# Optimization experiments

Measured on AMD Instinct MI355X. Metric: run time of the kernel, lower is better.

## Reference

```python
import jax, jax.numpy as jnp
import numpy as np

B, CIN, COUT, H, W = 8, 64, 64, 96, 96
K = 3
PAD = 1
BN_EPS = 1e-5


def conv2d(x, w, b):
    # plain 3x3 conv, stride 1, pad 1 (NCHW / OIHW)
    y = jax.lax.conv_general_dilated(
        x, w, window_strides=(1, 1), padding=[(PAD, PAD), (PAD, PAD)],
        dimension_numbers=("NCHW", "OIHW", "NCHW"))
    return y + b[None, :, None, None]


def setup_inputs() -> dict:
    key = jax.random.key(0)
    ks = jax.random.split(key, 6)
    s = 0.05  # small init so offsets stay near the regular grid (matches DCN zero-ish init)
    return {
        "x": jax.random.normal(ks[0], (B, CIN, H, W), jnp.float32),
        "offset_w": jax.random.normal(ks[1], (2 * K * K, CIN, K, K), jnp.float32) * s,
        "offset_b": jnp.zeros((2 * K * K,), jnp.float32),
        "mod_w": jax.random.normal(ks[2], (K * K, CIN, K, K), jnp.float32) * s,
        "mod_b": jnp.zeros((K * K,), jnp.float32),
        "weight": jax.random.normal(ks[3], (COUT, CIN, K, K), jnp.float32) * s,
        "bias": jax.random.normal(ks[4], (COUT,), jnp.float32) * s,
        "bn_gamma": jnp.ones((COUT,), jnp.float32),
        "bn_beta": jnp.zeros((COUT,), jnp.float32),
        "bn_mean": jnp.zeros((COUT,), jnp.float32),
        "bn_var": jnp.ones((COUT,), jnp.float32),
    }


def _deform_sample(xb, py, px):
    # xb: [C,H,W]; py, px: [K2,H,W] fractional sampling coords (zero outside image)
    y0 = jnp.floor(py)
    x0 = jnp.floor(px)
    dy = py - y0
    dx = px - x0

    def gather(yi, xi):
        valid = ((yi >= 0) & (yi < H) & (xi >= 0) & (xi < W)).astype(xb.dtype)
        yc = jnp.clip(yi, 0, H - 1).astype(jnp.int32)
        xc = jnp.clip(xi, 0, W - 1).astype(jnp.int32)
        return xb[:, yc, xc] * valid  # [C,K2,H,W]

    v00 = gather(y0, x0)
    v01 = gather(y0, x0 + 1.0)
    v10 = gather(y0 + 1.0, x0)
    v11 = gather(y0 + 1.0, x0 + 1.0)
    return (v00 * (1 - dy) * (1 - dx) + v01 * (1 - dy) * dx
            + v10 * dy * (1 - dx) + v11 * dy * dx)  # [C,K2,H,W]


def reference(x, offset_w, offset_b, mod_w, mod_b, weight, bias,
              bn_gamma, bn_beta, bn_mean, bn_var):
    # 1) predict offsets and modulation mask (DCNv2)
    offset = conv2d(x, offset_w, offset_b)                 # [B, 2*K2, H, W]
    modulator = 2.0 * jax.nn.sigmoid(conv2d(x, mod_w, mod_b))  # [B, K2, H, W]

    off = offset.reshape(B, K * K, 2, H, W)
    off_y, off_x = off[:, :, 0], off[:, :, 1]              # [B,K2,H,W]

    # 2) base sampling grid per kernel tap
    ky, kx = jnp.meshgrid(jnp.arange(K), jnp.arange(K), indexing="ij")
    base_y = (jnp.arange(H)[None, :, None] - PAD
              + ky.reshape(-1)[:, None, None]).astype(jnp.float32)  # [K2,H,1]
    base_x = (jnp.arange(W)[None, None, :] - PAD
              + kx.reshape(-1)[:, None, None]).astype(jnp.float32)  # [K2,1,W]
    py = base_y + off_y                                    # [B,K2,H,W]
    px = base_x + off_x

    # 3) bilinear gather at irregular positions, modulate per tap
    sampled = jax.vmap(_deform_sample)(x, py, px)          # [B,C,K2,H,W]
    sampled = sampled * modulator[:, None]                 # broadcast over C

    # 4) contract taps with the regular conv weight
    wk = weight.reshape(COUT, CIN, K * K)
    y = jnp.einsum("bckhw,ock->bohw", sampled, wk) + bias[None, :, None, None]

    # 5) BatchNorm (inference: running stats) + ReLU
    inv = bn_gamma / jnp.sqrt(bn_var + BN_EPS)
    y = (y - bn_mean[None, :, None, None]) * inv[None, :, None, None] \
        + bn_beta[None, :, None, None]
    return jax.nn.relu(y)
```

## Files before the change

### kernel.cpp

```cpp
#include <hip/hip_runtime.h>
#include <hip/hip_bf16.h>
#include <hip/hip_fp16.h>
#include <math.h>

#define BB 8
#define HH 96
#define WW 96
#define HW 9216
#define BN_EPS 1e-5f

typedef _Float16 f16x2 __attribute__((ext_vector_type(2)));
typedef _Float16 f16x8 __attribute__((ext_vector_type(8)));
typedef float f32x4 __attribute__((ext_vector_type(4)));

union HU  { _Float16 h; unsigned short u; };
union UH2 { unsigned u; f16x2 h; };
union U4H { uint4 u; f16x2 h2[4]; };

#define OFF_W4   0
#define SZ_W4    (BB*9*HW*16)
#define OFF_XT   (OFF_W4 + SZ_W4)
#define SZ_XT    (BB*HW*64*2)
#define OFF_XY   (OFF_XT + SZ_XT)
#define SZ_XY    (BB*9*HW*4)
#define OFF_WB   (OFF_XY + SZ_XY)
#define SZ_WB    (64*576*2)
#define OFF_WO   (OFF_WB + SZ_WB)
#define SZ_WO    (32*576*2)
#define OFF_BN   (OFF_WO + SZ_WO)
#define SZ_BN    (64*2*4)

__global__ __launch_bounds__(256) void prep_kernel(
    const float* __restrict__ weight, const float* __restrict__ offw,
    const float* __restrict__ modw,
    const float* __restrict__ bias, const float* __restrict__ gamma,
    const float* __restrict__ beta, const float* __restrict__ mean,
    const float* __restrict__ var,
    _Float16* __restrict__ wB, _Float16* __restrict__ wOff,
    float* __restrict__ bnS, float* __restrict__ bnB) {
  int tid = blockIdx.x * 256 + threadIdx.x;
  if (tid < 64 * 576) {
    int o = tid / 576, ck = tid % 576;
    int k = ck >> 6, c = ck & 63;
    wB[tid] = (_Float16)weight[o * 576 + c * 9 + k];
  }
  int t2 = tid - 64 * 576;
  if (t2 >= 0 && t2 < 32 * 576) {
    int oc = t2 / 576, kcol = t2 % 576;
    int kk = kcol >> 6, c = kcol & 63;
    float v = 0.f;
    if (oc < 18)      v = offw[(oc * 64 + c) * 9 + kk];
    else if (oc < 27) v = modw[((oc - 18) * 64 + c) * 9 + kk];
    wOff[t2] = (_Float16)v;
  }
  int t3 = tid - (64 * 576 + 32 * 576);
  if (t3 >= 0 && t3 < 64) {
    float inv = gamma[t3] * rsqrtf(var[t3] + BN_EPS);
    bnS[t3] = inv;
    bnB[t3] = (bias[t3] - mean[t3]) * inv + beta[t3];
  }
}

__global__ __launch_bounds__(256) void transpose_x_kernel(
    const float* __restrict__ x, _Float16* __restrict__ xT) {
  __shared__ float tile[64][65];
  int tid = threadIdx.x;
  int b = blockIdx.x & 7;
  int hwb = (blockIdx.x >> 3) * 64;
  int col = tid & 63, g = tid >> 6;
  float r[16];
#pragma unroll
  for (int it = 0; it < 16; ++it)
    r[it] = x[(b * 64 + it * 4 + g) * HW + hwb + col];
  __builtin_amdgcn_sched_barrier(0);
#pragma unroll
  for (int it = 0; it < 16; ++it)
    tile[it * 4 + g][col] = r[it];
  __syncthreads();
#pragma unroll
  for (int it = 0; it < 16; ++it) {
    int p = it * 4 + g;
    xT[(size_t)(b * HW + hwb + p) * 64 + col] = (_Float16)tile[col][p];
  }
}

__device__ __forceinline__ unsigned rep16(float w) {
  HU cv; cv.h = (_Float16)w;
  return 0x10001u * (unsigned)cv.u;
}

__global__ __launch_bounds__(256, 8) void conv_offsets_kernel(
    const _Float16* __restrict__ xTh, const _Float16* __restrict__ wOff,
    const float* __restrict__ offb, const float* __restrict__ modb,
    uint4* __restrict__ w4, unsigned* __restrict__ xy) {
  __shared__ __attribute__((aligned(16))) _Float16 sN[3 * 34 * 70];
  __shared__ float o_off[32 * 33];

  int tid = threadIdx.x;
  int lane = tid & 63;
  int wv = __builtin_amdgcn_readfirstlane(tid >> 6);

  int bi = blockIdx.x;
  int b = bi & 7, rem = bi >> 3;
  int h = rem / 3, w0 = (rem % 3) * 32;

  const _Float16* xb = xTh + (size_t)b * HW * 64;
  _Float16 sv[26];
#pragma unroll
  for (int i = 0; i < 26; ++i) {
    int p = wv + 4 * i;
    _Float16 v = (_Float16)0.f;
    if (p < 102) {
      int row = p / 34, col = p - row * 34;
      int y = h + row - 1, xx = w0 + col - 1;
      if ((y >= 0) && (y < HH) && (xx >= 0) && (xx < WW))
        v = xb[(size_t)(y * WW + xx) * 64 + lane];
    }
    sv[i] = v;
  }
  __builtin_amdgcn_sched_barrier(0);
#pragma unroll
  for (int i = 0; i < 26; ++i) {
    int p = wv + 4 * i;
    if (p < 102) {
      int row = p / 34, col = p - row * 34;
      sN[(row * 34 + col) * 70 + lane] = sv[i];
    }
  }
  __syncthreads();

  int r = lane & 15, g = lane >> 4;
  int mt = wv >> 1, nt = wv & 1;
  int px = mt * 16 + r;
  const _Float16* bp = wOff + (nt * 16 + r) * 576 + g * 8;
  f32x4 acc = {0.f, 0.f, 0.f, 0.f};
#pragma unroll
  for (int s = 0; s < 18; ++s) {
    int kk = s >> 1, ky = kk / 3, kx = kk - ky * 3;
    f16x8 a = *(const f16x8*)&sN[(ky * 34 + px + kx) * 70 + (s & 1) * 32 + g * 8];
    f16x8 bb = *(const f16x8*)(bp + s * 32);
    acc = __builtin_amdgcn_mfma_f32_16x16x32_f16(a, bb, acc, 0, 0, 0);
  }
#pragma unroll
  for (int j = 0; j < 4; ++j)
    o_off[(mt * 16 + g * 4 + j) * 33 + nt * 16 + r] = acc[j];
  __syncthreads();

  for (int it = tid; it < 288; it += 256) {
    int pxx = it & 31, k = it >> 5;
    int ky = k / 3, kx = k - ky * 3;
    int w = w0 + pxx;

    float offy = o_off[pxx * 33 + 2 * k]     + offb[2 * k];
    float offx = o_off[pxx * 33 + 2 * k + 1] + offb[2 * k + 1];
    float mod  = 2.f / (1.f + __expf(-(o_off[pxx * 33 + 18 + k] + modb[k])));

    float py  = (float)(h - 1 + ky) + offy;
    float px_ = (float)(w - 1 + kx) + offx;
    float y0f = floorf(py), x0f = floorf(px_);
    float dy = py - y0f, dx = px_ - x0f;
    int y0 = (int)y0f, x0 = (int)x0f;
    int y1 = y0 + 1, x1 = x0 + 1;
    bool vy0 = (y0 >= 0) && (y0 < HH), vy1 = (y1 >= 0) && (y1 < HH);
    bool vx0 = (x0 >= 0) && (x0 < WW), vx1 = (x1 >= 0) && (x1 < WW);
    float w00 = (vy0 && vx0) ? (1.f - dy) * (1.f - dx) * mod : 0.f;
    float w01 = (vy0 && vx1) ? (1.f - dy) * dx * mod : 0.f;
    float w10 = (vy1 && vx0) ? dy * (1.f - dx) * mod : 0.f;
    float w11 = (vy1 && vx1) ? dy * dx * mod : 0.f;
    int y0c = min(max(y0, 0), HH - 1), y1c = min(max(y1, 0), HH - 1);
    int x0c = min(max(x0, 0), WW - 1), x1c = min(max(x1, 0), WW - 1);
    unsigned pk = (unsigned)y0c | ((unsigned)y1c << 8) |
                  ((unsigned)x0c << 16) | ((unsigned)x1c << 24);
    int idx = (b * 9 + k) * HW + h * WW + w;
    w4[idx] = make_uint4(rep16(w00), rep16(w01), rep16(w10), rep16(w11));
    xy[idx] = pk;
  }
}

__global__ __launch_bounds__(256, 6) void dcn_main_kernel(
    const _Float16* __restrict__ xT,
    const uint4* __restrict__ w4pk, const unsigned* __restrict__ xy,
    const _Float16* __restrict__ wB,
    const float* __restrict__ bnS, const float* __restrict__ bnB,
    float* __restrict__ out) {
  __shared__ __attribute__((aligned(16))) _Float16 s_A[16 * 584];
  float* o_lds = (float*)s_A;

  int tid = threadIdx.x;
  int lane = tid & 63;
  int wv = __builtin_amdgcn_readfirstlane(tid >> 6);

  int bi = blockIdx.x;
  int b = bi & 7, t = bi >> 3;
  int h = t / 6, w0 = (t - (t / 6) * 6) * 16;
  int hwrow = h * WW + w0;

  const unsigned char* xbc = (const unsigned char*)(xT + (size_t)b * HW * 64);

  int pxi = lane >> 4;
  int cg  = lane & 15;
  int pl  = (wv << 2) + pxi;
  int hw  = hwrow + pl;
  unsigned cgB = (unsigned)(cg << 3);

  unsigned q[9];
#pragma unroll
  for (int k = 0; k < 9; ++k) q[k] = xy[(b * 9 + k) * HW + hw];

#pragma unroll
  for (int k = 0; k < 9; ++k) {
    uint4 wq = w4pk[(b * 9 + k) * HW + hw];
    unsigned qq = q[k];
    int y0 = qq & 255, y1 = (qq >> 8) & 255, x0 = (qq >> 16) & 255, x1 = qq >> 24;
    unsigned o00 = (unsigned)((y0 * WW + x0) << 7) + cgB;
    unsigned o01 = (unsigned)((y0 * WW + x1) << 7) + cgB;
    unsigned o10 = (unsigned)((y1 * WW + x0) << 7) + cgB;
    unsigned o11 = (unsigned)((y1 * WW + x1) << 7) + cgB;
    uint2 v0 = *(const uint2*)(xbc + o00);
    uint2 v1 = *(const uint2*)(xbc + o01);
    uint2 v2 = *(const uint2*)(xbc + o10);
    uint2 v3 = *(const uint2*)(xbc + o11);
    U4H W; W.u = wq;
    UH2 p0, p1, p2, p3, s0, s1;
    p0.u = v0.x; p1.u = v1.x; p2.u = v2.x; p3.u = v3.x;
    s0.h = p0.h * W.h2[0] + p1.h * W.h2[1] + p2.h * W.h2[2] + p3.h * W.h2[3];
    p0.u = v0.y; p1.u = v1.y; p2.u = v2.y; p3.u = v3.y;
    s1.h = p0.h * W.h2[0] + p1.h * W.h2[1] + p2.h * W.h2[2] + p3.h * W.h2[3];
    *(uint2*)&s_A[pl * 584 + k * 64 + (cg << 2)] = make_uint2(s0.u, s1.u);
  }
  __syncthreads();

  int r = lane & 15, g = lane >> 4;
  const _Float16* arow = s_A + r * 584 + g * 8;
  const _Float16* bp = wB + (wv * 16 + r) * 576 + g * 8;
  f32x4 accA = {0.f, 0.f, 0.f, 0.f}, accB = {0.f, 0.f, 0.f, 0.f};
#pragma unroll 3
  for (int s = 0; s < 18; s += 2) {
    f16x8 a0 = *(const f16x8*)(arow + s * 32);
    f16x8 b0 = *(const f16x8*)(bp + s * 32);
    f16x8 a1 = *(const f16x8*)(arow + s * 32 + 32);
    f16x8 b1 = *(const f16x8*)(bp + s * 32 + 32);
    accA = __builtin_amdgcn_mfma_f32_16x16x32_f16(a0, b0, accA, 0, 0, 0);
    accB = __builtin_amdgcn_mfma_f32_16x16x32_f16(a1, b1, accB, 0, 0, 0);
  }

  int o = wv * 16 + r;
  float sc = bnS[o], sh = bnB[o];
  __syncthreads();
#pragma unroll
  for (int j = 0; j < 4; ++j) {
    int px = g * 4 + j;
    o_lds[o * 20 + px] = fmaxf((accA[j] + accB[j]) * sc + sh, 0.f);
  }
  __syncthreads();

  int oo = tid >> 2, qd = tid & 3;
  float4 u = *(const float4*)&o_lds[oo * 20 + qd * 4];
  *(float4*)(out + (size_t)(b * 64 + oo) * HW + hwrow + qd * 4) = u;
}

extern "C" void kernel_launch(void* const* d_in, const int* in_sizes, int n_in,
                              void* d_out, int out_size, void* d_ws, size_t ws_size,
                              hipStream_t stream) {
  const float* x      = (const float*)d_in[0];
  const float* offw   = (const float*)d_in[1];
  const float* offb   = (const float*)d_in[2];
  const float* modw   = (const float*)d_in[3];
  const float* modb   = (const float*)d_in[4];
  const float* weight = (const float*)d_in[5];
  const float* bias   = (const float*)d_in[6];
  const float* gamma  = (const float*)d_in[7];
  const float* beta   = (const float*)d_in[8];
  const float* mean   = (const float*)d_in[9];
  const float* var    = (const float*)d_in[10];

  char* ws = (char*)d_ws;
  uint4*     w4    = (uint4*)(ws + OFF_W4);
  _Float16*  xTh   = (_Float16*)(ws + OFF_XT);
  unsigned*  xybuf = (unsigned*)(ws + OFF_XY);
  _Float16*  wB    = (_Float16*)(ws + OFF_WB);
  _Float16*  wOff  = (_Float16*)(ws + OFF_WO);
  float*     bnS   = (float*)(ws + OFF_BN);
  float*     bnB   = bnS + 64;

  prep_kernel<<<217, 256, 0, stream>>>(weight, offw, modw, bias, gamma, beta,
                                       mean, var, wB, wOff, bnS, bnB);
  transpose_x_kernel<<<1152, 256, 0, stream>>>(x, xTh);
  conv_offsets_kernel<<<2304, 256, 0, stream>>>(xTh, wOff, offb, modb, w4, xybuf);
  dcn_main_kernel<<<4608, 256, 0, stream>>>(xTh, w4, xybuf, wB, bnS, bnB,
                                            (float*)d_out);
}
```

Baseline: 108.4 us.

## Stage input window in LDS and loop over rows per block

Each block now covers a 16x16 output tile, loads a 31x32 pixel by 64 channel fp16 input window into LDS with direct global-to-LDS loads, and processes 16 rows sequentially. Bilinear gathers read from LDS when every lane's taps fall inside the window and fall back to global memory otherwise. The aim is to cut repeated global or L2 gather traffic. In exchange, occupancy drops to one large-LDS block per CU, and the grid shrinks to 288 blocks with serialized row iterations and extra barriers.

After: 230.3 us. 112% more time.

```diff
diff --git a/kernel.cpp b/kernel.cpp
--- a/kernel.cpp
+++ b/kernel.cpp
@@ -8,6 +8,8 @@
 #define WW 96
 #define HW 9216
 #define BN_EPS 1e-5f
+#define WR 31
+#define WC 32
 
 typedef _Float16 f16x2 __attribute__((ext_vector_type(2)));
 typedef _Float16 f16x8 __attribute__((ext_vector_type(8)));
@@ -16,6 +18,9 @@
 union HU  { _Float16 h; unsigned short u; };
 union UH2 { unsigned u; f16x2 h; };
 union U4H { uint4 u; f16x2 h2[4]; };
+
+typedef const __attribute__((address_space(1))) unsigned char g1_t;
+typedef __attribute__((address_space(3))) unsigned char l3_t;
 
 #define OFF_W4   0
 #define SZ_W4    (BB*9*HW*16)
@@ -177,12 +182,13 @@
   }
 }
 
-__global__ __launch_bounds__(256, 6) void dcn_main_kernel(
+__global__ __launch_bounds__(256, 1) void dcn_main_kernel(
     const _Float16* __restrict__ xT,
     const uint4* __restrict__ w4pk, const unsigned* __restrict__ xy,
     const _Float16* __restrict__ wB,
     const float* __restrict__ bnS, const float* __restrict__ bnB,
     float* __restrict__ out) {
+  __shared__ __attribute__((aligned(16))) _Float16 s_win[WR * WC * 64];
   __shared__ __attribute__((aligned(16))) _Float16 s_A[16 * 584];
   float* o_lds = (float*)s_A;
 
@@ -192,71 +198,107 @@
 
   int bi = blockIdx.x;
   int b = bi & 7, t = bi >> 3;
-  int h = t / 6, w0 = (t - (t / 6) * 6) * 16;
-  int hwrow = h * WW + w0;
+  int th = t / 6, tw = t - th * 6;
+  int h0 = th * 16, w0 = tw * 16;
 
   const unsigned char* xbc = (const unsigned char*)(xT + (size_t)b * HW * 64);
+
+  int y0w = h0 - 7;  y0w = y0w < 0 ? 0 : (y0w > HH - WR ? HH - WR : y0w);
+  int x0w = w0 - 8;  x0w = x0w < 0 ? 0 : (x0w > WW - WC ? WW - WC : x0w);
+  int yHi = y0w + WR - 1, xHi = x0w + WC - 1;
+
+#pragma unroll
+  for (int jj = 0; jj < 31; ++jj) {
+    int j = wv * 31 + jj;
+    int row = j >> 2, seg = j & 3;
+    unsigned srcOff = (unsigned)((((y0w + row) * WW + x0w) << 7) + (seg << 10));
+    __builtin_amdgcn_global_load_lds(
+        (g1_t*)(xbc + srcOff + (unsigned)(lane << 4)),
+        (l3_t*)s_win + (j << 10), 16, 0, 0);
+  }
+  asm volatile("s_waitcnt vmcnt(0)" ::: "memory");
+  __syncthreads();
 
   int pxi = lane >> 4;
   int cg  = lane & 15;
   int pl  = (wv << 2) + pxi;
-  int hw  = hwrow + pl;
   unsigned cgB = (unsigned)(cg << 3);
-
-  unsigned q[9];
-#pragma unroll
-  for (int k = 0; k < 9; ++k) q[k] = xy[(b * 9 + k) * HW + hw];
-
-#pragma unroll
-  for (int k = 0; k < 9; ++k) {
-    uint4 wq = w4pk[(b * 9 + k) * HW + hw];
-    unsigned qq = q[k];
-    int y0 = qq & 255, y1 = (qq >> 8) & 255, x0 = (qq >> 16) & 255, x1 = qq >> 24;
-    unsigned o00 = (unsigned)((y0 * WW + x0) << 7) + cgB;
-    unsigned o01 = (unsigned)((y0 * WW + x1) << 7) + cgB;
-    unsigned o10 = (unsigned)((y1 * WW + x0) << 7) + cgB;
-    unsigned o11 = (unsigned)((y1 * WW + x1) << 7) + cgB;
-    uint2 v0 = *(const uint2*)(xbc + o00);
-    uint2 v1 = *(const uint2*)(xbc + o01);
-    uint2 v2 = *(const uint2*)(xbc + o10);
-    uint2 v3 = *(const uint2*)(xbc + o11);
-    U4H W; W.u = wq;
-    UH2 p0, p1, p2, p3, s0, s1;
-    p0.u = v0.x; p1.u = v1.x; p2.u = v2.x; p3.u = v3.x;
-    s0.h = p0.h * W.h2[0] + p1.h * W.h2[1] + p2.h * W.h2[2] + p3.h * W.h2[3];
-    p0.u = v0.y; p1.u = v1.y; p2.u = v2.y; p3.u = v3.y;
-    s1.h = p0.h * W.h2[0] + p1.h * W.h2[1] + p2.h * W.h2[2] + p3.h * W.h2[3];
-    *(uint2*)&s_A[pl * 584 + k * 64 + (cg << 2)] = make_uint2(s0.u, s1.u);
-  }
-  __syncthreads();
+  const char* wp = (const char*)s_win;
 
   int r = lane & 15, g = lane >> 4;
-  const _Float16* arow = s_A + r * 584 + g * 8;
-  const _Float16* bp = wB + (wv * 16 + r) * 576 + g * 8;
-  f32x4 accA = {0.f, 0.f, 0.f, 0.f}, accB = {0.f, 0.f, 0.f, 0.f};
-#pragma unroll 3
-  for (int s = 0; s < 18; s += 2) {
-    f16x8 a0 = *(const f16x8*)(arow + s * 32);
-    f16x8 b0 = *(const f16x8*)(bp + s * 32);
-    f16x8 a1 = *(const f16x8*)(arow + s * 32 + 32);
-    f16x8 b1 = *(const f16x8*)(bp + s * 32 + 32);
-    accA = __builtin_amdgcn_mfma_f32_16x16x32_f16(a0, b0, accA, 0, 0, 0);
-    accB = __builtin_amdgcn_mfma_f32_16x16x32_f16(a1, b1, accB, 0, 0, 0);
-  }
-
   int o = wv * 16 + r;
   float sc = bnS[o], sh = bnB[o];
-  __syncthreads();
-#pragma unroll
-  for (int j = 0; j < 4; ++j) {
-    int px = g * 4 + j;
-    o_lds[o * 20 + px] = fmaxf((accA[j] + accB[j]) * sc + sh, 0.f);
-  }
-  __syncthreads();
-
-  int oo = tid >> 2, qd = tid & 3;
-  float4 u = *(const float4*)&o_lds[oo * 20 + qd * 4];
-  *(float4*)(out + (size_t)(b * 64 + oo) * HW + hwrow + qd * 4) = u;
+
+  for (int cc = 0; cc < 16; ++cc) {
+    int hwc = (h0 + cc) * WW + w0;
+    int hw  = hwc + pl;
+
+    unsigned q[9];
+#pragma unroll
+    for (int k = 0; k < 9; ++k) q[k] = xy[(b * 9 + k) * HW + hw];
+
+#pragma unroll
+    for (int k = 0; k < 9; ++k) {
+      uint4 wq = w4pk[(b * 9 + k) * HW + hw];
+      unsigned qq = q[k];
+      int y0 = qq & 255, y1 = (qq >> 8) & 255, x0 = (qq >> 16) & 255, x1 = qq >> 24;
+      uint2 v0, v1, v2, v3;
+      bool inw = (y0 >= y0w) && (y1 <= yHi) && (x0 >= x0w) && (x1 <= xHi);
+      if (__all(inw)) {
+        unsigned r00 = (unsigned)((((y0 - y0w) << 5) + (x0 - x0w)) << 7) + cgB;
+        unsigned r01 = (unsigned)((((y0 - y0w) << 5) + (x1 - x0w)) << 7) + cgB;
+        unsigned r10 = (unsigned)((((y1 - y0w) << 5) + (x0 - x0w)) << 7) + cgB;
+        unsigned r11 = (unsigned)((((y1 - y0w) << 5) + (x1 - x0w)) << 7) + cgB;
+        v0 = *(const uint2*)(wp + r00);
+        v1 = *(const uint2*)(wp + r01);
+        v2 = *(const uint2*)(wp + r10);
+        v3 = *(const uint2*)(wp + r11);
+      } else {
+        unsigned o00 = (unsigned)((y0 * WW + x0) << 7) + cgB;
+        unsigned o01 = (unsigned)((y0 * WW + x1) << 7) + cgB;
+        unsigned o10 = (unsigned)((y1 * WW + x0) << 7) + cgB;
+        unsigned o11 = (unsigned)((y1 * WW + x1) << 7) + cgB;
+        v0 = *(const uint2*)(xbc + o00);
+        v1 = *(const uint2*)(xbc + o01);
+        v2 = *(const uint2*)(xbc + o10);
+        v3 = *(const uint2*)(xbc + o11);
+      }
+      U4H W; W.u = wq;
+      UH2 p0, p1, p2, p3, s0, s1;
+      p0.u = v0.x; p1.u = v1.x; p2.u = v2.x; p3.u = v3.x;
+      s0.h = p0.h * W.h2[0] + p1.h * W.h2[1] + p2.h * W.h2[2] + p3.h * W.h2[3];
+      p0.u = v0.y; p1.u = v1.y; p2.u = v2.y; p3.u = v3.y;
+      s1.h = p0.h * W.h2[0] + p1.h * W.h2[1] + p2.h * W.h2[2] + p3.h * W.h2[3];
+      *(uint2*)&s_A[pl * 584 + k * 64 + (cg << 2)] = make_uint2(s0.u, s1.u);
+    }
+    __syncthreads();
+
+    const _Float16* arow = s_A + r * 584 + g * 8;
+    const _Float16* bp = wB + (wv * 16 + r) * 576 + g * 8;
+    f32x4 accA = {0.f, 0.f, 0.f, 0.f}, accB = {0.f, 0.f, 0.f, 0.f};
+#pragma unroll 3
+    for (int s = 0; s < 18; s += 2) {
+      f16x8 a0 = *(const f16x8*)(arow + s * 32);
+      f16x8 b0 = *(const f16x8*)(bp + s * 32);
+      f16x8 a1 = *(const f16x8*)(arow + s * 32 + 32);
+      f16x8 b1 = *(const f16x8*)(bp + s * 32 + 32);
+      accA = __builtin_amdgcn_mfma_f32_16x16x32_f16(a0, b0, accA, 0, 0, 0);
+      accB = __builtin_amdgcn_mfma_f32_16x16x32_f16(a1, b1, accB, 0, 0, 0);
+    }
+
+    __syncthreads();
+#pragma unroll
+    for (int j = 0; j < 4; ++j) {
+      int px = g * 4 + j;
+      o_lds[o * 20 + px] = fmaxf((accA[j] + accB[j]) * sc + sh, 0.f);
+    }
+    __syncthreads();
+
+    int oo = tid >> 2, qd = tid & 3;
+    float4 u = *(const float4*)&o_lds[oo * 20 + qd * 4];
+    *(float4*)(out + (size_t)(b * 64 + oo) * HW + hwc + qd * 4) = u;
+    __syncthreads();
+  }
 }
 
 extern "C" void kernel_launch(void* const* d_in, const int* in_sizes, int n_in,
@@ -287,6 +329,6 @@
                                        mean, var, wB, wOff, bnS, bnB);
   transpose_x_kernel<<<1152, 256, 0, stream>>>(x, xTh);
   conv_offsets_kernel<<<2304, 256, 0, stream>>>(xTh, wOff, offb, modb, w4, xybuf);
-  dcn_main_kernel<<<4608, 256, 0, stream>>>(xTh, w4, xybuf, wB, bnS, bnB,
-                                            (float*)d_out);
-}
+  dcn_main_kernel<<<288, 256, 0, stream>>>(xTh, w4, xybuf, wB, bnS, bnB,
+                                           (float*)d_out);
+}
```
